# Kernel optimization log

Measured on AMD Instinct MI355X. Metric: run time of the kernel, lower is better.

Reference implementation:

```python
import jax, jax.numpy as jnp
import numpy as np


def setup_inputs() -> dict:
    key = jax.random.key(0)
    ks = jax.random.split(key, 8)
    B, H, W = 32, 512, 512
    C_in, C, Cqk = 3, 512, 64  # 512, 512//8
    P = 16  # patch size / stride
    inputs_x = jax.random.normal(ks[0], (B, C_in, H, W), dtype=jnp.float32)
    # params initialized N(0, 0.1) per nn.init.normal_(m.weight, 0, 0.1); biases default zero-ish
    conv1_w = 0.1 * jax.random.normal(ks[1], (C, C_in, P, P), dtype=jnp.float32)
    wq = 0.1 * jax.random.normal(ks[2], (Cqk, C), dtype=jnp.float32)
    bq = jnp.zeros((Cqk,), dtype=jnp.float32)
    wk = 0.1 * jax.random.normal(ks[3], (Cqk, C), dtype=jnp.float32)
    bk = jnp.zeros((Cqk,), dtype=jnp.float32)
    wv = 0.1 * jax.random.normal(ks[4], (C, C), dtype=jnp.float32)
    bv = jnp.zeros((C,), dtype=jnp.float32)
    return {"inputs_x": inputs_x, "conv1_w": conv1_w, "wq": wq, "bq": bq,
            "wk": wk, "bk": bk, "wv": wv, "bv": bv}


def reference(inputs_x, conv1_w, wq, bq, wk, bk, wv, bv):
    P = conv1_w.shape[-1]
    # patchify conv: 3 -> 512, kernel 16, stride 16, no bias
    x = jax.lax.conv_general_dilated(
        inputs_x, conv1_w, window_strides=(P, P), padding='VALID',
        dimension_numbers=('NCHW', 'OIHW', 'NCHW'))  # [B, C, h, w]
    B, C, h, w = x.shape
    xf = x.reshape(B, C, h * w)  # [B, C, N]
    # 1x1 conv projections == channel matmuls (with bias)
    q = jnp.einsum('qc,bcn->bnq', wq, xf) + bq[None, None, :]   # [B, N, Cqk]
    k = jnp.einsum('qc,bcn->bqn', wk, xf) + bk[None, :, None]   # [B, Cqk, N]
    v = jnp.einsum('vc,bcn->bvn', wv, xf) + bv[None, :, None]   # [B, C, N]
    energy = jnp.einsum('bnq,bqm->bnm', q, k)                   # [B, N, N]
    energy = jnp.clip(energy, -1.0, 1.0)
    attention = jax.nn.softmax(energy, axis=-1)                 # softmax over last dim
    # out = bmm(V, attention^T): out[b,c,n] = sum_m v[b,c,m] * attn[b,n,m]
    out = jnp.einsum('bvm,bnm->bvn', v, attention)
    return out.reshape(B, C, h, w)
```

## Files before the change

kernel.cpp:

```cpp
#include <hip/hip_runtime.h>
#include <hip/hip_bf16.h>
#include <cstdint>

typedef unsigned short u16;
typedef unsigned int u32;
typedef __attribute__((ext_vector_type(8))) short bf16x8;
typedef __attribute__((ext_vector_type(4))) float f32x4;

#define B_   32
#define C_   512
#define CQK  64
#define NP   1024

#define LOFF(row, kb) (((row) << 7) + ((kb) ^ (((row) & 7) << 4)))

__device__ __forceinline__ u16 f2bf(float f) {
    union { __hip_bfloat16 b; u16 u; } cv;
    cv.b = __float2bfloat16(f);
    return cv.u;
}
__device__ __forceinline__ float bf2f(u16 h) {
    return __uint_as_float(((u32)h) << 16);
}

__device__ __forceinline__ void put16(u16* tile, int row, int kb, const u16* v) {
    char* p = (char*)tile;
    *(ushort4*)(p + LOFF(row, kb))          = *(const ushort4*)(v + 0);
    *(ushort4*)(p + LOFF(row, kb) + 8)      = *(const ushort4*)(v + 4);
    *(ushort4*)(p + LOFF(row, kb + 16))     = *(const ushort4*)(v + 8);
    *(ushort4*)(p + LOFF(row, kb + 16) + 8) = *(const ushort4*)(v + 12);
}

__device__ __forceinline__ void split16(const float* src, u16* h, u16* l) {
    float f[16];
    *(float4*)&f[0]  = *(const float4*)(src + 0);
    *(float4*)&f[4]  = *(const float4*)(src + 4);
    *(float4*)&f[8]  = *(const float4*)(src + 8);
    *(float4*)&f[12] = *(const float4*)(src + 12);
    #pragma unroll
    for (int i = 0; i < 16; ++i) {
        h[i] = f2bf(f[i]);
        l[i] = f2bf(f[i] - bf2f(h[i]));
    }
}
__device__ __forceinline__ void split8(const float* src, u16* h, u16* l) {
    float f[8];
    *(float4*)&f[0] = *(const float4*)(src);
    *(float4*)&f[4] = *(const float4*)(src + 4);
    #pragma unroll
    for (int i = 0; i < 8; ++i) {
        h[i] = f2bf(f[i]);
        l[i] = f2bf(f[i] - bf2f(h[i]));
    }
}

#define MFMA(a, b, c) __builtin_amdgcn_mfma_f32_16x16x32_bf16((a), (b), (c), 0, 0, 0)

__global__ __launch_bounds__(256) void prepack(
    const float* __restrict__ w1, const float* __restrict__ wq,
    const float* __restrict__ wk, const float* __restrict__ wv,
    u16* __restrict__ w1h, u16* __restrict__ w1l,
    u16* __restrict__ wqkh, u16* __restrict__ wqkl,
    u16* __restrict__ wvb)
{
    int t = blockIdx.x * 256 + threadIdx.x;
    if (t < 49152) {
        int e = t * 8;
        u16 h[8], l[8];
        split8(w1 + e, h, l);
        *(uint4*)(w1h + e) = *(const uint4*)h;
        *(uint4*)(w1l + e) = *(const uint4*)l;
    } else if (t < 57344) {
        int e = (t - 49152) * 8;
        const float* src = (e < 32768) ? (wq + e) : (wk + (e - 32768));
        u16 h[8], l[8];
        split8(src, h, l);
        *(uint4*)(wqkh + e) = *(const uint4*)h;
        *(uint4*)(wqkl + e) = *(const uint4*)l;
    } else if (t < 90112) {
        int e = (t - 57344) * 8;
        float f[8];
        *(float4*)&f[0] = *(const float4*)(wv + e);
        *(float4*)&f[4] = *(const float4*)(wv + e + 4);
        u16 h[8];
        #pragma unroll
        for (int i = 0; i < 8; ++i) h[i] = f2bf(f[i]);
        *(uint4*)(wvb + e) = *(const uint4*)h;
    }
}

__global__ __launch_bounds__(256) void convA(
    const float* __restrict__ x,
    const u16* __restrict__ w1h, const u16* __restrict__ w1l,
    u16* __restrict__ xhi, u16* __restrict__ xlo)
{
    __shared__ u16 Ah[128 * 64], Al[128 * 64], Bh[128 * 64], Bl[128 * 64];
    const int tid = threadIdx.x;
    const int bid = blockIdx.x;
    const int xcd = bid & 7, slot = bid >> 3;
    const int grp = slot >> 2, mt = slot & 3;
    const int gg = xcd * 32 + grp;
    const int b = gg >> 3, nt = gg & 7;
    const int n0 = nt * 128, ph0 = nt * 4;
    const int m0 = mt * 128;
    const int wid = tid >> 6, lane = tid & 63;
    const int wm = wid >> 1, wn = wid & 1;
    const int lr = lane & 15, lk = lane >> 4;

    f32x4 acc[4][4];
    #pragma unroll
    for (int i = 0; i < 4; ++i)
    #pragma unroll
    for (int j = 0; j < 4; ++j) acc[i][j] = f32x4{0.f, 0.f, 0.f, 0.f};

    for (int s = 0; s < 12; ++s) {
        const int k0 = s * 64;
        const int ci = s >> 2, ky0 = (s & 3) * 4;
        __syncthreads();
        #pragma unroll
        for (int it = 0; it < 4; ++it) {
            int idx = tid + it * 256;
            int row = idx >> 3, ch = idx & 7;
            size_t off = (size_t)(m0 + row) * 768 + k0 + ch * 8;
            *(uint4*)((char*)Ah + LOFF(row, ch * 16)) = *(const uint4*)(w1h + off);
            *(uint4*)((char*)Al + LOFF(row, ch * 16)) = *(const uint4*)(w1l + off);
        }
        #pragma unroll
        for (int it = 0; it < 2; ++it) {
            int u = tid + it * 256;
            int r = u >> 5, pw = u & 31;
            int phl = r >> 2, kyl = r & 3;
            int y = (ph0 + phl) * 16 + ky0 + kyl;
            const float* src = x + (((size_t)b * 3 + ci) * 512 + y) * 512 + pw * 16;
            int n = phl * 32 + pw;
            u16 h[16], l[16];
            split16(src, h, l);
            put16(Bh, n, kyl * 32, h);
            put16(Bl, n, kyl * 32, l);
        }
        __syncthreads();
        #pragma unroll
        for (int kk = 0; kk < 2; ++kk) {
            const int kb = kk * 64 + lk * 16;
            bf16x8 ah[4], al[4], bh[4], bl[4];
            #pragma unroll
            for (int mi = 0; mi < 4; ++mi) {
                int row = wm * 64 + mi * 16 + lr;
                ah[mi] = *(const bf16x8*)((const char*)Ah + LOFF(row, kb));
                al[mi] = *(const bf16x8*)((const char*)Al + LOFF(row, kb));
            }
            #pragma unroll
            for (int ni = 0; ni < 4; ++ni) {
                int row = wn * 64 + ni * 16 + lr;
                bh[ni] = *(const bf16x8*)((const char*)Bh + LOFF(row, kb));
                bl[ni] = *(const bf16x8*)((const char*)Bl + LOFF(row, kb));
            }
            #pragma unroll
            for (int mi = 0; mi < 4; ++mi)
            #pragma unroll
            for (int ni = 0; ni < 4; ++ni) {
                acc[mi][ni] = MFMA(ah[mi], bh[ni], acc[mi][ni]);
                acc[mi][ni] = MFMA(ah[mi], bl[ni], acc[mi][ni]);
                acc[mi][ni] = MFMA(al[mi], bh[ni], acc[mi][ni]);
            }
        }
    }
    #pragma unroll
    for (int mi = 0; mi < 4; ++mi)
    #pragma unroll
    for (int ni = 0; ni < 4; ++ni) {
        int c0 = m0 + wm * 64 + mi * 16 + lk * 4;
        int n  = n0 + wn * 64 + ni * 16 + lr;
        ushort4 h4, l4;
        float v0 = acc[mi][ni][0], v1 = acc[mi][ni][1];
        float v2 = acc[mi][ni][2], v3 = acc[mi][ni][3];
        h4.x = f2bf(v0); l4.x = f2bf(v0 - bf2f(h4.x));
        h4.y = f2bf(v1); l4.y = f2bf(v1 - bf2f(h4.y));
        h4.z = f2bf(v2); l4.z = f2bf(v2 - bf2f(h4.z));
        h4.w = f2bf(v3); l4.w = f2bf(v3 - bf2f(h4.w));
        size_t base = ((size_t)b * NP + n) * C_ + c0;
        *(ushort4*)&xhi[base] = h4;
        *(ushort4*)&xlo[base] = l4;
    }
}

__global__ __launch_bounds__(256) void projQK(
    const u16* __restrict__ xhi, const u16* __restrict__ xlo,
    const u16* __restrict__ wqkh, const u16* __restrict__ wqkl,
    const float* __restrict__ bq, const float* __restrict__ bk,
    u16* __restrict__ qhi, u16* __restrict__ qlo,
    u16* __restrict__ khi, u16* __restrict__ klo)
{
    __shared__ u16 Wh[128 * 64], Wl[128 * 64], Xh[64 * 64], Xl[64 * 64];
    __shared__ float biasS[128];
    const int tid = threadIdx.x;
    const int b = blockIdx.x >> 4, n0 = (blockIdx.x & 15) * 64;
    const int wid = tid >> 6, lane = tid & 63;
    const int wm = wid >> 1, wn = wid & 1;
    const int lr = lane & 15, lk = lane >> 4;
    if (tid < 128) biasS[tid] = (tid < 64) ? bq[tid] : bk[tid - 64];

    f32x4 acc[4][2];
    #pragma unroll
    for (int i = 0; i < 4; ++i) {
        acc[i][0] = f32x4{0.f, 0.f, 0.f, 0.f};
        acc[i][1] = f32x4{0.f, 0.f, 0.f, 0.f};
    }

    for (int s = 0; s < 8; ++s) {
        const int k0 = s * 64;
        __syncthreads();
        #pragma unroll
        for (int it = 0; it < 4; ++it) {
            int idx = tid + it * 256;
            int row = idx >> 3, ch = idx & 7;
            size_t off = (size_t)row * C_ + k0 + ch * 8;
            *(uint4*)((char*)Wh + LOFF(row, ch * 16)) = *(const uint4*)(wqkh + off);
            *(uint4*)((char*)Wl + LOFF(row, ch * 16)) = *(const uint4*)(wqkl + off);
        }
        #pragma unroll
        for (int it = 0; it < 4; ++it) {
            int idx = tid + it * 256;
            int sel = idx >> 9, u = idx & 511;
            int row = u >> 3, ch = u & 7;
            const u16* src = (sel ? xlo : xhi) + ((size_t)b * NP + n0 + row) * C_ + k0 + ch * 8;
            uint4 v = *(const uint4*)src;
            *(uint4*)((char*)(sel ? Xl : Xh) + LOFF(row, ch * 16)) = v;
        }
        __syncthreads();
        #pragma unroll
        for (int kk = 0; kk < 2; ++kk) {
            const int kb = kk * 64 + lk * 16;
            bf16x8 ah[4], al[4], bh[2], bl[2];
            #pragma unroll
            for (int mi = 0; mi < 4; ++mi) {
                int row = wm * 64 + mi * 16 + lr;
                ah[mi] = *(const bf16x8*)((const char*)Wh + LOFF(row, kb));
                al[mi] = *(const bf16x8*)((const char*)Wl + LOFF(row, kb));
            }
            #pragma unroll
            for (int ni = 0; ni < 2; ++ni) {
                int row = wn * 32 + ni * 16 + lr;
                bh[ni] = *(const bf16x8*)((const char*)Xh + LOFF(row, kb));
                bl[ni] = *(const bf16x8*)((const char*)Xl + LOFF(row, kb));
            }
            #pragma unroll
            for (int mi = 0; mi < 4; ++mi)
            #pragma unroll
            for (int ni = 0; ni < 2; ++ni) {
                acc[mi][ni] = MFMA(ah[mi], bh[ni], acc[mi][ni]);
                acc[mi][ni] = MFMA(ah[mi], bl[ni], acc[mi][ni]);
                acc[mi][ni] = MFMA(al[mi], bh[ni], acc[mi][ni]);
            }
        }
    }
    #pragma unroll
    for (int mi = 0; mi < 4; ++mi)
    #pragma unroll
    for (int ni = 0; ni < 2; ++ni) {
        int j0 = wm * 64 + mi * 16 + lk * 4;
        int n  = n0 + wn * 32 + ni * 16 + lr;
        float4 bb = *(float4*)&biasS[j0];
        float v0 = acc[mi][ni][0] + bb.x, v1 = acc[mi][ni][1] + bb.y;
        float v2 = acc[mi][ni][2] + bb.z, v3 = acc[mi][ni][3] + bb.w;
        ushort4 h4, l4;
        h4.x = f2bf(v0); l4.x = f2bf(v0 - bf2f(h4.x));
        h4.y = f2bf(v1); l4.y = f2bf(v1 - bf2f(h4.y));
        h4.z = f2bf(v2); l4.z = f2bf(v2 - bf2f(h4.z));
        h4.w = f2bf(v3); l4.w = f2bf(v3 - bf2f(h4.w));
        if (wm == 0) {
            size_t base = ((size_t)b * NP + n) * CQK + j0;
            *(ushort4*)&qhi[base] = h4;
            *(ushort4*)&qlo[base] = l4;
        } else {
            size_t base = ((size_t)b * NP + n) * CQK + (j0 - 64);
            *(ushort4*)&khi[base] = h4;
            *(ushort4*)&klo[base] = l4;
        }
    }
}

__global__ __launch_bounds__(256) void projV(
    const u16* __restrict__ xhi, const u16* __restrict__ wvb,
    const float* __restrict__ bv, u16* __restrict__ vws)
{
    __shared__ u16 Xt[128 * 64], Wt[128 * 64];
    __shared__ float biasS[128];
    const int tid = threadIdx.x;
    const int bid = blockIdx.x;
    const int xcd = bid & 7, slot = bid >> 3;
    const int b = xcd * 4 + (slot >> 5);
    const int r = slot & 31;
    const int n0 = (r >> 2) * 128;
    const int c0 = (r & 3) * 128;
    const int wid = tid >> 6, lane = tid & 63;
    const int wm = wid >> 1, wn = wid & 1;
    const int lr = lane & 15, lk = lane >> 4;
    if (tid < 128) biasS[tid] = bv[c0 + tid];

    f32x4 acc[4][4];
    #pragma unroll
    for (int i = 0; i < 4; ++i)
    #pragma unroll
    for (int j = 0; j < 4; ++j) acc[i][j] = f32x4{0.f, 0.f, 0.f, 0.f};

    for (int s = 0; s < 8; ++s) {
        const int k0 = s * 64;
        __syncthreads();
        #pragma unroll
        for (int it = 0; it < 4; ++it) {
            int idx = tid + it * 256;
            int row = idx >> 3, ch = idx & 7;
            const u16* src = xhi + ((size_t)b * NP + n0 + row) * C_ + k0 + ch * 8;
            uint4 v = *(const uint4*)src;
            *(uint4*)((char*)Xt + LOFF(row, ch * 16)) = v;
        }
        #pragma unroll
        for (int it = 0; it < 4; ++it) {
            int idx = tid + it * 256;
            int row = idx >> 3, ch = idx & 7;
            const u16* src = wvb + (size_t)(c0 + row) * C_ + k0 + ch * 8;
            *(uint4*)((char*)Wt + LOFF(row, ch * 16)) = *(const uint4*)src;
        }
        __syncthreads();
        #pragma unroll
        for (int kk = 0; kk < 2; ++kk) {
            const int kb = kk * 64 + lk * 16;
            bf16x8 a[4], bfr[4];
            #pragma unroll
            for (int mi = 0; mi < 4; ++mi) {
                int row = wm * 64 + mi * 16 + lr;
                a[mi] = *(const bf16x8*)((const char*)Xt + LOFF(row, kb));
            }
            #pragma unroll
            for (int ni = 0; ni < 4; ++ni) {
                int row = wn * 64 + ni * 16 + lr;
                bfr[ni] = *(const bf16x8*)((const char*)Wt + LOFF(row, kb));
            }
            #pragma unroll
            for (int mi = 0; mi < 4; ++mi)
            #pragma unroll
            for (int ni = 0; ni < 4; ++ni)
                acc[mi][ni] = MFMA(a[mi], bfr[ni], acc[mi][ni]);
        }
    }
    #pragma unroll
    for (int mi = 0; mi < 4; ++mi)
    #pragma unroll
    for (int ni = 0; ni < 4; ++ni) {
        int nr0 = n0 + wm * 64 + mi * 16 + lk * 4;
        int c   = c0 + wn * 64 + ni * 16 + lr;
        float bias = biasS[wn * 64 + ni * 16 + lr];
        ushort4 h4;
        h4.x = f2bf(acc[mi][ni][0] + bias);
        h4.y = f2bf(acc[mi][ni][1] + bias);
        h4.z = f2bf(acc[mi][ni][2] + bias);
        h4.w = f2bf(acc[mi][ni][3] + bias);
        *(ushort4*)&vws[((size_t)b * C_ + c) * NP + nr0] = h4;
    }
}

__global__ __launch_bounds__(256) void attnE(
    const u16* __restrict__ qhi, const u16* __restrict__ qlo,
    const u16* __restrict__ khi, const u16* __restrict__ klo,
    u16* __restrict__ Pws, float* __restrict__ Zws)
{
    __shared__ u16 Kh[64 * 64], Kl[64 * 64], Qh[64 * 64], Ql[64 * 64];
    __shared__ float zs[64];
    const int tid = threadIdx.x;
    const int b = blockIdx.x >> 4, n0 = (blockIdx.x & 15) * 64;
    const int wid = tid >> 6, lane = tid & 63;
    const int wr = wid >> 1, wn = wid & 1;
    const int lr = lane & 15, lk = lane >> 4;
    if (tid < 64) zs[tid] = 0.f;

    #pragma unroll
    for (int it = 0; it < 4; ++it) {
        int idx = tid + it * 256;
        int sel = idx >> 9, u = idx & 511;
        int row = u >> 3, ch = u & 7;
        const u16* src = (sel ? qlo : qhi) + ((size_t)b * NP + n0 + row) * CQK + ch * 8;
        uint4 v = *(const uint4*)src;
        *(uint4*)((char*)(sel ? Ql : Qh) + LOFF(row, ch * 16)) = v;
    }
    __syncthreads();
    bf16x8 qh[2][2], ql[2][2];
    #pragma unroll
    for (int ni = 0; ni < 2; ++ni)
    #pragma unroll
    for (int kk = 0; kk < 2; ++kk) {
        int row = wn * 32 + ni * 16 + lr;
        int kb = kk * 64 + lk * 16;
        qh[ni][kk] = *(const bf16x8*)((const char*)Qh + LOFF(row, kb));
        ql[ni][kk] = *(const bf16x8*)((const char*)Ql + LOFF(row, kb));
    }

    float z[2] = {0.f, 0.f};
    for (int ms = 0; ms < 16; ++ms) {
        const int m0 = ms * 64;
        __syncthreads();
        #pragma unroll
        for (int it = 0; it < 4; ++it) {
            int idx = tid + it * 256;
            int sel = idx >> 9, u = idx & 511;
            int row = u >> 3, ch = u & 7;
            const u16* src = (sel ? klo : khi) + ((size_t)b * NP + m0 + row) * CQK + ch * 8;
            uint4 v = *(const uint4*)src;
            *(uint4*)((char*)(sel ? Kl : Kh) + LOFF(row, ch * 16)) = v;
        }
        __syncthreads();
        f32x4 e[2][2];
        #pragma unroll
        for (int i = 0; i < 2; ++i) {
            e[i][0] = f32x4{0.f, 0.f, 0.f, 0.f};
            e[i][1] = f32x4{0.f, 0.f, 0.f, 0.f};
        }
        #pragma unroll
        for (int kk = 0; kk < 2; ++kk) {
            const int kb = kk * 64 + lk * 16;
            bf16x8 ah[2], al[2];
            #pragma unroll
            for (int mi = 0; mi < 2; ++mi) {
                int row = wr * 32 + mi * 16 + lr;
                ah[mi] = *(const bf16x8*)((const char*)Kh + LOFF(row, kb));
                al[mi] = *(const bf16x8*)((const char*)Kl + LOFF(row, kb));
            }
            #pragma unroll
            for (int mi = 0; mi < 2; ++mi)
            #pragma unroll
            for (int ni = 0; ni < 2; ++ni) {
                e[mi][ni] = MFMA(ah[mi], qh[ni][kk], e[mi][ni]);
                e[mi][ni] = MFMA(ah[mi], ql[ni][kk], e[mi][ni]);
                e[mi][ni] = MFMA(al[mi], qh[ni][kk], e[mi][ni]);
            }
        }
        #pragma unroll
        for (int mi = 0; mi < 2; ++mi)
        #pragma unroll
        for (int ni = 0; ni < 2; ++ni) {
            int n  = n0 + wn * 32 + ni * 16 + lr;
            int mg = m0 + wr * 32 + mi * 16 + lk * 4;
            float e0 = __expf(fminf(fmaxf(e[mi][ni][0], -1.f), 1.f));
            float e1 = __expf(fminf(fmaxf(e[mi][ni][1], -1.f), 1.f));
            float e2 = __expf(fminf(fmaxf(e[mi][ni][2], -1.f), 1.f));
            float e3 = __expf(fminf(fmaxf(e[mi][ni][3], -1.f), 1.f));
            z[ni] += e0 + e1 + e2 + e3;
            ushort4 p4;
            p4.x = f2bf(e0); p4.y = f2bf(e1); p4.z = f2bf(e2); p4.w = f2bf(e3);
            *(ushort4*)&Pws[((size_t)b * NP + n) * NP + mg] = p4;
        }
    }
    z[0] += __shfl_xor(z[0], 16); z[0] += __shfl_xor(z[0], 32);
    z[1] += __shfl_xor(z[1], 16); z[1] += __shfl_xor(z[1], 32);
    if (lk == 0) {
        atomicAdd(&zs[wn * 32 + lr], z[0]);
        atomicAdd(&zs[wn * 32 + 16 + lr], z[1]);
    }
    __syncthreads();
    if (tid < 64) Zws[(size_t)b * NP + n0 + tid] = zs[tid];
}

__global__ __launch_bounds__(256) void pvOut(
    const u16* __restrict__ Pws, const u16* __restrict__ vws,
    const float* __restrict__ Zws, float* __restrict__ out)
{
    __shared__ u16 Pt[128 * 64], Vt[128 * 64];
    __shared__ float zinv[128];
    const int tid = threadIdx.x;
    const int bid = blockIdx.x;
    const int xcd = bid & 7, slot = bid >> 3;
    const int b = xcd * 4 + (slot >> 5);
    const int r = slot & 31;
    const int n0 = (r >> 2) * 128;
    const int c0 = (r & 3) * 128;
    const int wid = tid >> 6, lane = tid & 63;
    const int wm = wid >> 1, wn = wid & 1;
    const int lr = lane & 15, lk = lane >> 4;
    if (tid < 128) zinv[tid] = 1.0f / Zws[(size_t)b * NP + n0 + tid];

    f32x4 acc[4][4];
    #pragma unroll
    for (int i = 0; i < 4; ++i)
    #pragma unroll
    for (int j = 0; j < 4; ++j) acc[i][j] = f32x4{0.f, 0.f, 0.f, 0.f};

    for (int s = 0; s < 16; ++s) {
        const int m0 = s * 64;
        __syncthreads();
        #pragma unroll
        for (int it = 0; it < 4; ++it) {
            int idx = tid + it * 256;
            int row = idx >> 3, ch = idx & 7;
            const u16* src = Pws + ((size_t)b * NP + n0 + row) * NP + m0 + ch * 8;
            uint4 v = *(const uint4*)src;
            *(uint4*)((char*)Pt + LOFF(row, ch * 16)) = v;
        }
        #pragma unroll
        for (int it = 0; it < 4; ++it) {
            int idx = tid + it * 256;
            int row = idx >> 3, ch = idx & 7;
            const u16* src = vws + ((size_t)b * C_ + c0 + row) * NP + m0 + ch * 8;
            uint4 v = *(const uint4*)src;
            *(uint4*)((char*)Vt + LOFF(row, ch * 16)) = v;
        }
        __syncthreads();
        #pragma unroll
        for (int kk = 0; kk < 2; ++kk) {
            const int kb = kk * 64 + lk * 16;
            bf16x8 a[4], bfr[4];
            #pragma unroll
            for (int mi = 0; mi < 4; ++mi) {
                int row = wm * 64 + mi * 16 + lr;
                a[mi] = *(const bf16x8*)((const char*)Pt + LOFF(row, kb));
            }
            #pragma unroll
            for (int ni = 0; ni < 4; ++ni) {
                int row = wn * 64 + ni * 16 + lr;
                bfr[ni] = *(const bf16x8*)((const char*)Vt + LOFF(row, kb));
            }
            #pragma unroll
            for (int mi = 0; mi < 4; ++mi)
            #pragma unroll
            for (int ni = 0; ni < 4; ++ni)
                acc[mi][ni] = MFMA(a[mi], bfr[ni], acc[mi][ni]);
        }
    }
    #pragma unroll
    for (int mi = 0; mi < 4; ++mi)
    #pragma unroll
    for (int ni = 0; ni < 4; ++ni) {
        int nl0 = wm * 64 + mi * 16 + lk * 4;
        int c   = c0 + wn * 64 + ni * 16 + lr;
        float4 zi = *(float4*)&zinv[nl0];
        float4 o;
        o.x = acc[mi][ni][0] * zi.x;
        o.y = acc[mi][ni][1] * zi.y;
        o.z = acc[mi][ni][2] * zi.z;
        o.w = acc[mi][ni][3] * zi.w;
        *(float4*)&out[((size_t)b * C_ + c) * NP + n0 + nl0] = o;
    }
}

extern "C" void kernel_launch(void* const* d_in, const int* in_sizes, int n_in,
                              void* d_out, int out_size, void* d_ws, size_t ws_size,
                              hipStream_t stream) {
    const float* x  = (const float*)d_in[0];
    const float* w1 = (const float*)d_in[1];
    const float* wq = (const float*)d_in[2];
    const float* bq = (const float*)d_in[3];
    const float* wk = (const float*)d_in[4];
    const float* bk = (const float*)d_in[5];
    const float* wv = (const float*)d_in[6];
    const float* bv = (const float*)d_in[7];
    float* out = (float*)d_out;

    char* ws = (char*)d_ws;
    u16* xhi = (u16*)(ws + 0);
    u16* xlo = (u16*)(ws + 33554432ULL);
    u16* Pws = (u16*)(ws + 0);
    u16* qhi = (u16*)(ws + 67108864ULL);
    u16* qlo = (u16*)(ws + 71303168ULL);
    u16* khi = (u16*)(ws + 75497472ULL);
    u16* klo = (u16*)(ws + 79691776ULL);
    u16* vws = (u16*)(ws + 83886080ULL);
    float* Zws = (float*)(ws + 117440512ULL);

    char* sc = (char*)d_out;
    u16* w1h  = (u16*)(sc + 0);
    u16* w1l  = (u16*)(sc + 786432);
    u16* wqkh = (u16*)(sc + 1572864);
    u16* wqkl = (u16*)(sc + 1703936);
    u16* wvb  = (u16*)(sc + 1835008);

    prepack<<<352, 256, 0, stream>>>(w1, wq, wk, wv, w1h, w1l, wqkh, wqkl, wvb);
    convA <<<1024, 256, 0, stream>>>(x, w1h, w1l, xhi, xlo);
    projQK<<<512,  256, 0, stream>>>(xhi, xlo, wqkh, wqkl, bq, bk, qhi, qlo, khi, klo);
    projV <<<1024, 256, 0, stream>>>(xhi, wvb, bv, vws);
    attnE <<<512,  256, 0, stream>>>(qhi, qlo, khi, klo, Pws, Zws);
    pvOut <<<1024, 256, 0, stream>>>(Pws, vws, Zws, out);
}
```

Baseline: 383.5 us.

## Fold patch-conv weights into Q/K/V projections and fuse projection kernels

Precomputes composed weights Wq·W1, Wk·W1 and Wv·W1 (768-wide) in small setup kernels, then computes Q, K and V directly from the raw input patches in one fused projAll kernel. This removes the intermediate x feature map (hi/lo bf16, written and re-read) and the separate conv, projQK and projV kernels. The fused kernel's K dimension drops from 768+512 per stage to 768, so V uses fewer FLOPs overall. The trade-off is that precision changes: V is computed from single bf16 input and weights without the compensation terms, and the composed weights are rounded again.

```diff
diff --git a/kernel.cpp b/kernel.cpp
--- a/kernel.cpp
+++ b/kernel.cpp
@@ -43,66 +43,44 @@
         l[i] = f2bf(f[i] - bf2f(h[i]));
     }
 }
-__device__ __forceinline__ void split8(const float* src, u16* h, u16* l) {
-    float f[8];
-    *(float4*)&f[0] = *(const float4*)(src);
-    *(float4*)&f[4] = *(const float4*)(src + 4);
-    #pragma unroll
-    for (int i = 0; i < 8; ++i) {
-        h[i] = f2bf(f[i]);
-        l[i] = f2bf(f[i] - bf2f(h[i]));
-    }
+__device__ __forceinline__ void cvt16(const float* src, u16* h) {
+    float f[16];
+    *(float4*)&f[0]  = *(const float4*)(src + 0);
+    *(float4*)&f[4]  = *(const float4*)(src + 4);
+    *(float4*)&f[8]  = *(const float4*)(src + 8);
+    *(float4*)&f[12] = *(const float4*)(src + 12);
+    #pragma unroll
+    for (int i = 0; i < 16; ++i) h[i] = f2bf(f[i]);
 }
 
 #define MFMA(a, b, c) __builtin_amdgcn_mfma_f32_16x16x32_bf16((a), (b), (c), 0, 0, 0)
 
-__global__ __launch_bounds__(256) void prepack(
-    const float* __restrict__ w1, const float* __restrict__ wq,
-    const float* __restrict__ wk, const float* __restrict__ wv,
-    u16* __restrict__ w1h, u16* __restrict__ w1l,
-    u16* __restrict__ wqkh, u16* __restrict__ wqkl,
-    u16* __restrict__ wvb)
+__global__ __launch_bounds__(256) void transposeW1(
+    const float* __restrict__ w1, float* __restrict__ w1T)
 {
-    int t = blockIdx.x * 256 + threadIdx.x;
-    if (t < 49152) {
-        int e = t * 8;
-        u16 h[8], l[8];
-        split8(w1 + e, h, l);
-        *(uint4*)(w1h + e) = *(const uint4*)h;
-        *(uint4*)(w1l + e) = *(const uint4*)l;
-    } else if (t < 57344) {
-        int e = (t - 49152) * 8;
-        const float* src = (e < 32768) ? (wq + e) : (wk + (e - 32768));
-        u16 h[8], l[8];
-        split8(src, h, l);
-        *(uint4*)(wqkh + e) = *(const uint4*)h;
-        *(uint4*)(wqkl + e) = *(const uint4*)l;
-    } else if (t < 90112) {
-        int e = (t - 57344) * 8;
-        float f[8];
-        *(float4*)&f[0] = *(const float4*)(wv + e);
-        *(float4*)&f[4] = *(const float4*)(wv + e + 4);
-        u16 h[8];
-        #pragma unroll
-        for (int i = 0; i < 8; ++i) h[i] = f2bf(f[i]);
-        *(uint4*)(wvb + e) = *(const uint4*)h;
-    }
-}
-
-__global__ __launch_bounds__(256) void convA(
-    const float* __restrict__ x,
-    const u16* __restrict__ w1h, const u16* __restrict__ w1l,
-    u16* __restrict__ xhi, u16* __restrict__ xlo)
+    __shared__ float t[32][33];
+    const int tx = threadIdx.x & 31, ty = threadIdx.x >> 5;
+    const int k0 = blockIdx.x * 32, c0 = blockIdx.y * 32;
+    #pragma unroll
+    for (int j = 0; j < 4; ++j)
+        t[ty + j * 8][tx] = w1[(size_t)(c0 + ty + j * 8) * 768 + k0 + tx];
+    __syncthreads();
+    #pragma unroll
+    for (int j = 0; j < 4; ++j)
+        w1T[(size_t)(k0 + ty + j * 8) * 512 + c0 + tx] = t[tx][ty + j * 8];
+}
+
+__global__ __launch_bounds__(256) void composeW(
+    const float* __restrict__ w1T,
+    const float* __restrict__ wq, const float* __restrict__ wk,
+    const float* __restrict__ wv,
+    u16* __restrict__ wqk1h, u16* __restrict__ wqk1l, u16* __restrict__ wv1b)
 {
     __shared__ u16 Ah[128 * 64], Al[128 * 64], Bh[128 * 64], Bl[128 * 64];
     const int tid = threadIdx.x;
-    const int bid = blockIdx.x;
-    const int xcd = bid & 7, slot = bid >> 3;
-    const int grp = slot >> 2, mt = slot & 3;
-    const int gg = xcd * 32 + grp;
-    const int b = gg >> 3, nt = gg & 7;
-    const int n0 = nt * 128, ph0 = nt * 4;
-    const int m0 = mt * 128;
+    const int m0 = blockIdx.x * 128;
+    const int jn0 = blockIdx.y * 128;
+    const bool qk = (blockIdx.y == 0);
     const int wid = tid >> 6, lane = tid & 63;
     const int wm = wid >> 1, wn = wid & 1;
     const int lr = lane & 15, lk = lane >> 4;
@@ -113,250 +91,265 @@
     #pragma unroll
     for (int j = 0; j < 4; ++j) acc[i][j] = f32x4{0.f, 0.f, 0.f, 0.f};
 
+    for (int s = 0; s < 8; ++s) {
+        const int k0 = s * 64;
+        __syncthreads();
+        #pragma unroll
+        for (int it = 0; it < 2; ++it) {
+            int u = tid + it * 256;
+            int row = u >> 2, q = u & 3;
+            const float* asrc = w1T + (size_t)(m0 + row) * 512 + k0 + q * 16;
+            int j = jn0 + row;
+            const float* bsrc = (j < 64 ? wq + (size_t)j * 512
+                               : j < 128 ? wk + (size_t)(j - 64) * 512
+                                         : wv + (size_t)(j - 128) * 512) + k0 + q * 16;
+            if (qk) {
+                u16 h[16], l[16];
+                split16(asrc, h, l);
+                put16(Ah, row, q * 32, h);
+                put16(Al, row, q * 32, l);
+                split16(bsrc, h, l);
+                put16(Bh, row, q * 32, h);
+                put16(Bl, row, q * 32, l);
+            } else {
+                u16 h[16];
+                cvt16(asrc, h);
+                put16(Ah, row, q * 32, h);
+                cvt16(bsrc, h);
+                put16(Bh, row, q * 32, h);
+            }
+        }
+        __syncthreads();
+        #pragma unroll
+        for (int kk = 0; kk < 2; ++kk) {
+            const int kb = kk * 64 + lk * 16;
+            bf16x8 ah[4], al[4], bh[4], bl[4];
+            #pragma unroll
+            for (int mi = 0; mi < 4; ++mi) {
+                int row = wm * 64 + mi * 16 + lr;
+                ah[mi] = *(const bf16x8*)((const char*)Ah + LOFF(row, kb));
+                if (qk) al[mi] = *(const bf16x8*)((const char*)Al + LOFF(row, kb));
+            }
+            #pragma unroll
+            for (int ni = 0; ni < 4; ++ni) {
+                int row = wn * 64 + ni * 16 + lr;
+                bh[ni] = *(const bf16x8*)((const char*)Bh + LOFF(row, kb));
+                if (qk) bl[ni] = *(const bf16x8*)((const char*)Bl + LOFF(row, kb));
+            }
+            #pragma unroll
+            for (int mi = 0; mi < 4; ++mi)
+            #pragma unroll
+            for (int ni = 0; ni < 4; ++ni) {
+                acc[mi][ni] = MFMA(ah[mi], bh[ni], acc[mi][ni]);
+                if (qk) {
+                    acc[mi][ni] = MFMA(ah[mi], bl[ni], acc[mi][ni]);
+                    acc[mi][ni] = MFMA(al[mi], bh[ni], acc[mi][ni]);
+                }
+            }
+        }
+    }
+    #pragma unroll
+    for (int mi = 0; mi < 4; ++mi)
+    #pragma unroll
+    for (int ni = 0; ni < 4; ++ni) {
+        int kd0 = m0 + wm * 64 + mi * 16 + lk * 4;
+        int j   = jn0 + wn * 64 + ni * 16 + lr;
+        float v0 = acc[mi][ni][0], v1 = acc[mi][ni][1];
+        float v2 = acc[mi][ni][2], v3 = acc[mi][ni][3];
+        if (j < 128) {
+            ushort4 h4, l4;
+            h4.x = f2bf(v0); l4.x = f2bf(v0 - bf2f(h4.x));
+            h4.y = f2bf(v1); l4.y = f2bf(v1 - bf2f(h4.y));
+            h4.z = f2bf(v2); l4.z = f2bf(v2 - bf2f(h4.z));
+            h4.w = f2bf(v3); l4.w = f2bf(v3 - bf2f(h4.w));
+            *(ushort4*)&wqk1h[(size_t)j * 768 + kd0] = h4;
+            *(ushort4*)&wqk1l[(size_t)j * 768 + kd0] = l4;
+        } else {
+            ushort4 h4;
+            h4.x = f2bf(v0); h4.y = f2bf(v1); h4.z = f2bf(v2); h4.w = f2bf(v3);
+            *(ushort4*)&wv1b[(size_t)(j - 128) * 768 + kd0] = h4;
+        }
+    }
+}
+
+__global__ __launch_bounds__(256) void projAll(
+    const float* __restrict__ x,
+    const u16* __restrict__ wqk1h, const u16* __restrict__ wqk1l,
+    const u16* __restrict__ wv1b,
+    const float* __restrict__ bq, const float* __restrict__ bk,
+    const float* __restrict__ bv,
+    u16* __restrict__ qhi, u16* __restrict__ qlo,
+    u16* __restrict__ khi, u16* __restrict__ klo,
+    u16* __restrict__ vws)
+{
+    __shared__ u16 lds[4 * 128 * 64];
+    u16* Ah = lds;
+    u16* Al = lds + 8192;
+    u16* Bh = lds + 16384;
+    u16* Bl = lds + 24576;
+    __shared__ float biasS[128];
+
+    const int tid = threadIdx.x;
+    const int bid = blockIdx.x;
+    const int xcd = bid & 7, slot = bid >> 3;
+    const int b = xcd * 4 + (slot / 40);
+    const int r = slot % 40;
+    const int nt = r / 5, mt = r % 5;
+    const int n0 = nt * 128, ph0 = nt * 4;
+    const int wid = tid >> 6, lane = tid & 63;
+    const int wm = wid >> 1, wn = wid & 1;
+    const int lr = lane & 15, lk = lane >> 4;
+
+    const int cv0 = (mt - 1) * 128;
+    if (mt == 0) {
+        if (tid < 128) biasS[tid] = (tid < 64) ? bq[tid] : bk[tid - 64];
+    } else {
+        if (tid < 128) biasS[tid] = bv[cv0 + tid];
+    }
+
+    f32x4 acc[4][4];
+    #pragma unroll
+    for (int i = 0; i < 4; ++i)
+    #pragma unroll
+    for (int j = 0; j < 4; ++j) acc[i][j] = f32x4{0.f, 0.f, 0.f, 0.f};
+
     for (int s = 0; s < 12; ++s) {
         const int k0 = s * 64;
         const int ci = s >> 2, ky0 = (s & 3) * 4;
         __syncthreads();
-        #pragma unroll
-        for (int it = 0; it < 4; ++it) {
-            int idx = tid + it * 256;
-            int row = idx >> 3, ch = idx & 7;
-            size_t off = (size_t)(m0 + row) * 768 + k0 + ch * 8;
-            *(uint4*)((char*)Ah + LOFF(row, ch * 16)) = *(const uint4*)(w1h + off);
-            *(uint4*)((char*)Al + LOFF(row, ch * 16)) = *(const uint4*)(w1l + off);
-        }
-        #pragma unroll
-        for (int it = 0; it < 2; ++it) {
-            int u = tid + it * 256;
-            int r = u >> 5, pw = u & 31;
-            int phl = r >> 2, kyl = r & 3;
-            int y = (ph0 + phl) * 16 + ky0 + kyl;
-            const float* src = x + (((size_t)b * 3 + ci) * 512 + y) * 512 + pw * 16;
-            int n = phl * 32 + pw;
-            u16 h[16], l[16];
-            split16(src, h, l);
-            put16(Bh, n, kyl * 32, h);
-            put16(Bl, n, kyl * 32, l);
-        }
-        __syncthreads();
-        #pragma unroll
-        for (int kk = 0; kk < 2; ++kk) {
-            const int kb = kk * 64 + lk * 16;
-            bf16x8 ah[4], al[4], bh[4], bl[4];
-            #pragma unroll
-            for (int mi = 0; mi < 4; ++mi) {
-                int row = wm * 64 + mi * 16 + lr;
-                ah[mi] = *(const bf16x8*)((const char*)Ah + LOFF(row, kb));
-                al[mi] = *(const bf16x8*)((const char*)Al + LOFF(row, kb));
-            }
-            #pragma unroll
-            for (int ni = 0; ni < 4; ++ni) {
-                int row = wn * 64 + ni * 16 + lr;
-                bh[ni] = *(const bf16x8*)((const char*)Bh + LOFF(row, kb));
-                bl[ni] = *(const bf16x8*)((const char*)Bl + LOFF(row, kb));
-            }
-            #pragma unroll
-            for (int mi = 0; mi < 4; ++mi)
-            #pragma unroll
-            for (int ni = 0; ni < 4; ++ni) {
-                acc[mi][ni] = MFMA(ah[mi], bh[ni], acc[mi][ni]);
-                acc[mi][ni] = MFMA(ah[mi], bl[ni], acc[mi][ni]);
-                acc[mi][ni] = MFMA(al[mi], bh[ni], acc[mi][ni]);
-            }
-        }
-    }
-    #pragma unroll
-    for (int mi = 0; mi < 4; ++mi)
-    #pragma unroll
-    for (int ni = 0; ni < 4; ++ni) {
-        int c0 = m0 + wm * 64 + mi * 16 + lk * 4;
-        int n  = n0 + wn * 64 + ni * 16 + lr;
-        ushort4 h4, l4;
-        float v0 = acc[mi][ni][0], v1 = acc[mi][ni][1];
-        float v2 = acc[mi][ni][2], v3 = acc[mi][ni][3];
-        h4.x = f2bf(v0); l4.x = f2bf(v0 - bf2f(h4.x));
-        h4.y = f2bf(v1); l4.y = f2bf(v1 - bf2f(h4.y));
-        h4.z = f2bf(v2); l4.z = f2bf(v2 - bf2f(h4.z));
-        h4.w = f2bf(v3); l4.w = f2bf(v3 - bf2f(h4.w));
-        size_t base = ((size_t)b * NP + n) * C_ + c0;
-        *(ushort4*)&xhi[base] = h4;
-        *(ushort4*)&xlo[base] = l4;
-    }
-}
-
-__global__ __launch_bounds__(256) void projQK(
-    const u16* __restrict__ xhi, const u16* __restrict__ xlo,
-    const u16* __restrict__ wqkh, const u16* __restrict__ wqkl,
-    const float* __restrict__ bq, const float* __restrict__ bk,
-    u16* __restrict__ qhi, u16* __restrict__ qlo,
-    u16* __restrict__ khi, u16* __restrict__ klo)
-{
-    __shared__ u16 Wh[128 * 64], Wl[128 * 64], Xh[64 * 64], Xl[64 * 64];
-    __shared__ float biasS[128];
-    const int tid = threadIdx.x;
-    const int b = blockIdx.x >> 4, n0 = (blockIdx.x & 15) * 64;
-    const int wid = tid >> 6, lane = tid & 63;
-    const int wm = wid >> 1, wn = wid & 1;
-    const int lr = lane & 15, lk = lane >> 4;
-    if (tid < 128) biasS[tid] = (tid < 64) ? bq[tid] : bk[tid - 64];
-
-    f32x4 acc[4][2];
-    #pragma unroll
-    for (int i = 0; i < 4; ++i) {
-        acc[i][0] = f32x4{0.f, 0.f, 0.f, 0.f};
-        acc[i][1] = f32x4{0.f, 0.f, 0.f, 0.f};
-    }
-
-    for (int s = 0; s < 8; ++s) {
-        const int k0 = s * 64;
-        __syncthreads();
-        #pragma unroll
-        for (int it = 0; it < 4; ++it) {
-            int idx = tid + it * 256;
-            int row = idx >> 3, ch = idx & 7;
-            size_t off = (size_t)row * C_ + k0 + ch * 8;
-            *(uint4*)((char*)Wh + LOFF(row, ch * 16)) = *(const uint4*)(wqkh + off);
-            *(uint4*)((char*)Wl + LOFF(row, ch * 16)) = *(const uint4*)(wqkl + off);
-        }
-        #pragma unroll
-        for (int it = 0; it < 4; ++it) {
-            int idx = tid + it * 256;
-            int sel = idx >> 9, u = idx & 511;
-            int row = u >> 3, ch = u & 7;
-            const u16* src = (sel ? xlo : xhi) + ((size_t)b * NP + n0 + row) * C_ + k0 + ch * 8;
-            uint4 v = *(const uint4*)src;
-            *(uint4*)((char*)(sel ? Xl : Xh) + LOFF(row, ch * 16)) = v;
-        }
-        __syncthreads();
-        #pragma unroll
-        for (int kk = 0; kk < 2; ++kk) {
-            const int kb = kk * 64 + lk * 16;
-            bf16x8 ah[4], al[4], bh[2], bl[2];
-            #pragma unroll
-            for (int mi = 0; mi < 4; ++mi) {
-                int row = wm * 64 + mi * 16 + lr;
-                ah[mi] = *(const bf16x8*)((const char*)Wh + LOFF(row, kb));
-                al[mi] = *(const bf16x8*)((const char*)Wl + LOFF(row, kb));
-            }
-            #pragma unroll
-            for (int ni = 0; ni < 2; ++ni) {
-                int row = wn * 32 + ni * 16 + lr;
-                bh[ni] = *(const bf16x8*)((const char*)Xh + LOFF(row, kb));
-                bl[ni] = *(const bf16x8*)((const char*)Xl + LOFF(row, kb));
-            }
-            #pragma unroll
-            for (int mi = 0; mi < 4; ++mi)
-            #pragma unroll
-            for (int ni = 0; ni < 2; ++ni) {
-                acc[mi][ni] = MFMA(ah[mi], bh[ni], acc[mi][ni]);
-                acc[mi][ni] = MFMA(ah[mi], bl[ni], acc[mi][ni]);
-                acc[mi][ni] = MFMA(al[mi], bh[ni], acc[mi][ni]);
-            }
-        }
-    }
-    #pragma unroll
-    for (int mi = 0; mi < 4; ++mi)
-    #pragma unroll
-    for (int ni = 0; ni < 2; ++ni) {
-        int j0 = wm * 64 + mi * 16 + lk * 4;
-        int n  = n0 + wn * 32 + ni * 16 + lr;
-        float4 bb = *(float4*)&biasS[j0];
-        float v0 = acc[mi][ni][0] + bb.x, v1 = acc[mi][ni][1] + bb.y;
-        float v2 = acc[mi][ni][2] + bb.z, v3 = acc[mi][ni][3] + bb.w;
-        ushort4 h4, l4;
-        h4.x = f2bf(v0); l4.x = f2bf(v0 - bf2f(h4.x));
-        h4.y = f2bf(v1); l4.y = f2bf(v1 - bf2f(h4.y));
-        h4.z = f2bf(v2); l4.z = f2bf(v2 - bf2f(h4.z));
-        h4.w = f2bf(v3); l4.w = f2bf(v3 - bf2f(h4.w));
-        if (wm == 0) {
-            size_t base = ((size_t)b * NP + n) * CQK + j0;
-            *(ushort4*)&qhi[base] = h4;
-            *(ushort4*)&qlo[base] = l4;
+        if (mt == 0) {
+            #pragma unroll
+            for (int it = 0; it < 4; ++it) {
+                int idx = tid + it * 256;
+                int row = idx >> 3, ch = idx & 7;
+                size_t off = (size_t)row * 768 + k0 + ch * 8;
+                *(uint4*)((char*)Ah + LOFF(row, ch * 16)) = *(const uint4*)(wqk1h + off);
+                *(uint4*)((char*)Al + LOFF(row, ch * 16)) = *(const uint4*)(wqk1l + off);
+            }
+            #pragma unroll
+            for (int it = 0; it < 2; ++it) {
+                int u = tid + it * 256;
+                int rr = u >> 5, pw = u & 31;
+                int phl = rr >> 2, kyl = rr & 3;
+                int y = (ph0 + phl) * 16 + ky0 + kyl;
+                const float* src = x + (((size_t)b * 3 + ci) * 512 + y) * 512 + pw * 16;
+                int n = phl * 32 + pw;
+                u16 h[16], l[16];
+                split16(src, h, l);
+                put16(Bh, n, kyl * 32, h);
+                put16(Bl, n, kyl * 32, l);
+            }
         } else {
-            size_t base = ((size_t)b * NP + n) * CQK + (j0 - 64);
-            *(ushort4*)&khi[base] = h4;
-            *(ushort4*)&klo[base] = l4;
-        }
-    }
-}
-
-__global__ __launch_bounds__(256) void projV(
-    const u16* __restrict__ xhi, const u16* __restrict__ wvb,
-    const float* __restrict__ bv, u16* __restrict__ vws)
-{
-    __shared__ u16 Xt[128 * 64], Wt[128 * 64];
-    __shared__ float biasS[128];
-    const int tid = threadIdx.x;
-    const int bid = blockIdx.x;
-    const int xcd = bid & 7, slot = bid >> 3;
-    const int b = xcd * 4 + (slot >> 5);
-    const int r = slot & 31;
-    const int n0 = (r >> 2) * 128;
-    const int c0 = (r & 3) * 128;
-    const int wid = tid >> 6, lane = tid & 63;
-    const int wm = wid >> 1, wn = wid & 1;
-    const int lr = lane & 15, lk = lane >> 4;
-    if (tid < 128) biasS[tid] = bv[c0 + tid];
-
-    f32x4 acc[4][4];
-    #pragma unroll
-    for (int i = 0; i < 4; ++i)
-    #pragma unroll
-    for (int j = 0; j < 4; ++j) acc[i][j] = f32x4{0.f, 0.f, 0.f, 0.f};
-
-    for (int s = 0; s < 8; ++s) {
-        const int k0 = s * 64;
-        __syncthreads();
-        #pragma unroll
-        for (int it = 0; it < 4; ++it) {
-            int idx = tid + it * 256;
-            int row = idx >> 3, ch = idx & 7;
-            const u16* src = xhi + ((size_t)b * NP + n0 + row) * C_ + k0 + ch * 8;
-            uint4 v = *(const uint4*)src;
-            *(uint4*)((char*)Xt + LOFF(row, ch * 16)) = v;
-        }
-        #pragma unroll
-        for (int it = 0; it < 4; ++it) {
-            int idx = tid + it * 256;
-            int row = idx >> 3, ch = idx & 7;
-            const u16* src = wvb + (size_t)(c0 + row) * C_ + k0 + ch * 8;
-            *(uint4*)((char*)Wt + LOFF(row, ch * 16)) = *(const uint4*)src;
-        }
-        __syncthreads();
-        #pragma unroll
-        for (int kk = 0; kk < 2; ++kk) {
-            const int kb = kk * 64 + lk * 16;
-            bf16x8 a[4], bfr[4];
-            #pragma unroll
-            for (int mi = 0; mi < 4; ++mi) {
-                int row = wm * 64 + mi * 16 + lr;
-                a[mi] = *(const bf16x8*)((const char*)Xt + LOFF(row, kb));
-            }
-            #pragma unroll
-            for (int ni = 0; ni < 4; ++ni) {
-                int row = wn * 64 + ni * 16 + lr;
-                bfr[ni] = *(const bf16x8*)((const char*)Wt + LOFF(row, kb));
-            }
-            #pragma unroll
-            for (int mi = 0; mi < 4; ++mi)
-            #pragma unroll
-            for (int ni = 0; ni < 4; ++ni)
-                acc[mi][ni] = MFMA(a[mi], bfr[ni], acc[mi][ni]);
-        }
-    }
-    #pragma unroll
-    for (int mi = 0; mi < 4; ++mi)
-    #pragma unroll
-    for (int ni = 0; ni < 4; ++ni) {
-        int nr0 = n0 + wm * 64 + mi * 16 + lk * 4;
-        int c   = c0 + wn * 64 + ni * 16 + lr;
-        float bias = biasS[wn * 64 + ni * 16 + lr];
-        ushort4 h4;
-        h4.x = f2bf(acc[mi][ni][0] + bias);
-        h4.y = f2bf(acc[mi][ni][1] + bias);
-        h4.z = f2bf(acc[mi][ni][2] + bias);
-        h4.w = f2bf(acc[mi][ni][3] + bias);
-        *(ushort4*)&vws[((size_t)b * C_ + c) * NP + nr0] = h4;
+            #pragma unroll
+            for (int it = 0; it < 4; ++it) {
+                int idx = tid + it * 256;
+                int row = idx >> 3, ch = idx & 7;
+                size_t off = (size_t)(cv0 + row) * 768 + k0 + ch * 8;
+                *(uint4*)((char*)Ah + LOFF(row, ch * 16)) = *(const uint4*)(wv1b + off);
+            }
+            #pragma unroll
+            for (int it = 0; it < 2; ++it) {
+                int u = tid + it * 256;
+                int rr = u >> 5, pw = u & 31;
+                int phl = rr >> 2, kyl = rr & 3;
+                int y = (ph0 + phl) * 16 + ky0 + kyl;
+                const float* src = x + (((size_t)b * 3 + ci) * 512 + y) * 512 + pw * 16;
+                int n = phl * 32 + pw;
+                u16 h[16];
+                cvt16(src, h);
+                put16(Bh, n, kyl * 32, h);
+            }
+        }
+        __syncthreads();
+        if (mt == 0) {
+            #pragma unroll
+            for (int kk = 0; kk < 2; ++kk) {
+                const int kb = kk * 64 + lk * 16;
+                bf16x8 ah[4], al[4], bh[4], bl[4];
+                #pragma unroll
+                for (int mi = 0; mi < 4; ++mi) {
+                    int row = wm * 64 + mi * 16 + lr;
+                    ah[mi] = *(const bf16x8*)((const char*)Ah + LOFF(row, kb));
+                    al[mi] = *(const bf16x8*)((const char*)Al + LOFF(row, kb));
+                }
+                #pragma unroll
+                for (int ni = 0; ni < 4; ++ni) {
+                    int row = wn * 64 + ni * 16 + lr;
+                    bh[ni] = *(const bf16x8*)((const char*)Bh + LOFF(row, kb));
+                    bl[ni] = *(const bf16x8*)((const char*)Bl + LOFF(row, kb));
+                }
+                #pragma unroll
+                for (int mi = 0; mi < 4; ++mi)
+                #pragma unroll
+                for (int ni = 0; ni < 4; ++ni) {
+                    acc[mi][ni] = MFMA(ah[mi], bh[ni], acc[mi][ni]);
+                    acc[mi][ni] = MFMA(ah[mi], bl[ni], acc[mi][ni]);
+                    acc[mi][ni] = MFMA(al[mi], bh[ni], acc[mi][ni]);
+                }
+            }
+        } else {
+            #pragma unroll
+            for (int kk = 0; kk < 2; ++kk) {
+                const int kb = kk * 64 + lk * 16;
+                bf16x8 a[4], bfr[4];
+                #pragma unroll
+                for (int mi = 0; mi < 4; ++mi) {
+                    int row = wm * 64 + mi * 16 + lr;
+                    a[mi] = *(const bf16x8*)((const char*)Bh + LOFF(row, kb));
+                }
+                #pragma unroll
+                for (int ni = 0; ni < 4; ++ni) {
+                    int row = wn * 64 + ni * 16 + lr;
+                    bfr[ni] = *(const bf16x8*)((const char*)Ah + LOFF(row, kb));
+                }
+                #pragma unroll
+                for (int mi = 0; mi < 4; ++mi)
+                #pragma unroll
+                for (int ni = 0; ni < 4; ++ni)
+                    acc[mi][ni] = MFMA(a[mi], bfr[ni], acc[mi][ni]);
+            }
+        }
+    }
+    if (mt == 0) {
+        #pragma unroll
+        for (int mi = 0; mi < 4; ++mi)
+        #pragma unroll
+        for (int ni = 0; ni < 4; ++ni) {
+            int j0 = wm * 64 + mi * 16 + lk * 4;
+            int n  = n0 + wn * 64 + ni * 16 + lr;
+            float4 bb = *(float4*)&biasS[j0];
+            float v0 = acc[mi][ni][0] + bb.x, v1 = acc[mi][ni][1] + bb.y;
+            float v2 = acc[mi][ni][2] + bb.z, v3 = acc[mi][ni][3] + bb.w;
+            ushort4 h4, l4;
+            h4.x = f2bf(v0); l4.x = f2bf(v0 - bf2f(h4.x));
+            h4.y = f2bf(v1); l4.y = f2bf(v1 - bf2f(h4.y));
+            h4.z = f2bf(v2); l4.z = f2bf(v2 - bf2f(h4.z));
+            h4.w = f2bf(v3); l4.w = f2bf(v3 - bf2f(h4.w));
+            if (j0 < 64) {
+                size_t base = ((size_t)b * NP + n) * CQK + j0;
+                *(ushort4*)&qhi[base] = h4;
+                *(ushort4*)&qlo[base] = l4;
+            } else {
+                size_t base = ((size_t)b * NP + n) * CQK + (j0 - 64);
+                *(ushort4*)&khi[base] = h4;
+                *(ushort4*)&klo[base] = l4;
+            }
+        }
+    } else {
+        #pragma unroll
+        for (int mi = 0; mi < 4; ++mi)
+        #pragma unroll
+        for (int ni = 0; ni < 4; ++ni) {
+            int nr0 = n0 + wm * 64 + mi * 16 + lk * 4;
+            int c   = cv0 + wn * 64 + ni * 16 + lr;
+            float bias = biasS[wn * 64 + ni * 16 + lr];
+            ushort4 h4;
+            h4.x = f2bf(acc[mi][ni][0] + bias);
+            h4.y = f2bf(acc[mi][ni][1] + bias);
+            h4.z = f2bf(acc[mi][ni][2] + bias);
+            h4.w = f2bf(acc[mi][ni][3] + bias);
+            *(ushort4*)&vws[((size_t)b * C_ + c) * NP + nr0] = h4;
+        }
     }
 }
 
@@ -555,8 +548,6 @@
     float* out = (float*)d_out;
 
     char* ws = (char*)d_ws;
-    u16* xhi = (u16*)(ws + 0);
-    u16* xlo = (u16*)(ws + 33554432ULL);
     u16* Pws = (u16*)(ws + 0);
     u16* qhi = (u16*)(ws + 67108864ULL);
     u16* qlo = (u16*)(ws + 71303168ULL);
@@ -566,16 +557,15 @@
     float* Zws = (float*)(ws + 117440512ULL);
 
     char* sc = (char*)d_out;
-    u16* w1h  = (u16*)(sc + 0);
-    u16* w1l  = (u16*)(sc + 786432);
-    u16* wqkh = (u16*)(sc + 1572864);
-    u16* wqkl = (u16*)(sc + 1703936);
-    u16* wvb  = (u16*)(sc + 1835008);
-
-    prepack<<<352, 256, 0, stream>>>(w1, wq, wk, wv, w1h, w1l, wqkh, wqkl, wvb);
-    convA <<<1024, 256, 0, stream>>>(x, w1h, w1l, xhi, xlo);
-    projQK<<<512,  256, 0, stream>>>(xhi, xlo, wqkh, wqkl, bq, bk, qhi, qlo, khi, klo);
-    projV <<<1024, 256, 0, stream>>>(xhi, wvb, bv, vws);
+    float* w1T  = (float*)(sc + 0);
+    u16* wqk1h  = (u16*)(sc + 1572864);
+    u16* wqk1l  = (u16*)(sc + 1769472);
+    u16* wv1b   = (u16*)(sc + 1966080);
+
+    transposeW1<<<dim3(24, 16), 256, 0, stream>>>(w1, w1T);
+    composeW<<<dim3(6, 5), 256, 0, stream>>>(w1T, wq, wk, wv, wqk1h, wqk1l, wv1b);
+    projAll<<<1280, 256, 0, stream>>>(x, wqk1h, wqk1l, wv1b, bq, bk, bv,
+                                      qhi, qlo, khi, klo, vws);
     attnE <<<512,  256, 0, stream>>>(qhi, qlo, khi, klo, Pws, Zws);
     pvOut <<<1024, 256, 0, stream>>>(Pws, vws, Zws, out);
 }
```

New measurement: 369.9 us. 1.04x faster.
